# Performance work log

Measured on AMD Instinct MI355X. Metric: run time of the kernel, lower is better.

The kernel has to match this reference:

```python
import jax, jax.numpy as jnp
import numpy as np

H = 16        # attention heads
KVH = 4       # kv heads (GQA)
D = 128       # qk head_dim = qk_nope(64) + qk_rope(64)
ROPE = 64     # rotary sub-dim
VCH = 128     # v_channels
HID = 2048    # hidden size
E = 8         # routed experts
K = 2         # top-k
EPS = 1e-6
THETA = 10000.0


def rmsnorm(x, w):
    return x * jax.lax.rsqrt(jnp.mean(x * x, axis=-1, keepdims=True) + EPS) * w


def apply_rope(x, pos):
    # x: [T, h, ROPE]; rotate-half convention on the rope sub-dim
    half = ROPE // 2
    inv_freq = 1.0 / (THETA ** (jnp.arange(half, dtype=jnp.float32) / half))
    ang = pos.astype(jnp.float32)[:, None] * inv_freq          # [T, half]
    cos = jnp.cos(ang)[:, None, :]
    sin = jnp.sin(ang)[:, None, :]
    x1, x2 = x[..., :half], x[..., half:]
    return jnp.concatenate([x1 * cos - x2 * sin, x1 * sin + x2 * cos], axis=-1)


def swiglu(x, w_gate, w_up, w_down):
    return (jax.nn.silu(x @ w_gate) * (x @ w_up)) @ w_down


def setup_inputs() -> dict:
    key = jax.random.key(0)
    ks = jax.random.split(key, 16)
    T = 2048
    sc = 0.02
    n = lambda k, s: jax.random.normal(k, s, dtype=jnp.float32) * sc
    return {
        "x": jax.random.normal(ks[0], (T, HID), dtype=jnp.float32),
        "positions": jnp.arange(T, dtype=jnp.int32),
        "ln1_w": jnp.ones((HID,), jnp.float32),
        "qkv_w": n(ks[1], (HID, H * D + KVH * D + KVH * VCH)),
        "qkv_b": n(ks[2], (H * D + KVH * D + KVH * VCH,)),
        "k_ln_w": jnp.ones((D,), jnp.float32),
        "o_w": n(ks[3], (H * VCH, HID)),
        "ln2_w": jnp.ones((HID,), jnp.float32),
        "router_w": n(ks[4], (HID, E)),
        "w1": n(ks[5], (E, HID, 512)),
        "w2": n(ks[6], (E, 512, HID)),
        "w3": n(ks[7], (E, HID, 512)),
        "sw1": n(ks[8], (HID, 1024)),
        "sw2": n(ks[9], (1024, HID)),
        "sw3": n(ks[10], (HID, 1024)),
    }


def reference(x, positions, ln1_w, qkv_w, qkv_b, k_ln_w, o_w, ln2_w,
              router_w, w1, w2, w3, sw1, sw2, sw3):
    T = x.shape[0]
    # --- attention block ---
    h = rmsnorm(x, ln1_w)
    qkv = h @ qkv_w + qkv_b
    q = qkv[:, : H * D].reshape(T, H, D)
    k = qkv[:, H * D : H * D + KVH * D].reshape(T, KVH, D)
    v = qkv[:, H * D + KVH * D :].reshape(T, KVH, VCH)
    k = rmsnorm(k, k_ln_w)  # per-head k_layernorm over head_dim
    # rope applied to the trailing qk_rope_dim of q/k
    q = jnp.concatenate([q[..., : D - ROPE], apply_rope(q[..., D - ROPE :], positions)], -1)
    k = jnp.concatenate([k[..., : D - ROPE], apply_rope(k[..., D - ROPE :], positions)], -1)
    rep = H // KVH
    kf = jnp.repeat(k, rep, axis=1)   # [T, H, D]
    vf = jnp.repeat(v, rep, axis=1)   # [T, H, VCH]
    scale = D ** -0.5
    scores = jnp.einsum("qhd,khd->hqk", q, kf) * scale
    causal = jnp.tril(jnp.ones((T, T), dtype=bool))
    scores = jnp.where(causal[None], scores, jnp.float32(-1e30))
    p = jax.nn.softmax(scores, axis=-1)
    attn = jnp.einsum("hqk,khv->qhv", p, vf).reshape(T, H * VCH)
    x = x + attn @ o_w
    # --- MoE block: shared expert + top-k routed experts ---
    h2 = rmsnorm(x, ln2_w)
    probs = jax.nn.softmax(h2 @ router_w, axis=-1)            # [T, E]
    topw, topi = jax.lax.top_k(probs, K)
    topw = topw / jnp.sum(topw, axis=-1, keepdims=True)        # renormalize top-k
    combine = jnp.sum(jax.nn.one_hot(topi, E, dtype=h2.dtype) * topw[..., None], axis=1)  # [T, E]
    moe = swiglu(h2, sw1, sw3, sw2)                            # shared expert
    for e in range(E):  # small fixed expert count
        moe = moe + combine[:, e : e + 1] * swiglu(h2, w1[e], w3[e], w2[e])
    return x + moe
```

## Files before the change

kernel.cpp:

```cpp
#include <hip/hip_runtime.h>


typedef _Float16 half_t;
typedef _Float16 half8 __attribute__((ext_vector_type(8)));
typedef float    f32x4 __attribute__((ext_vector_type(4)));
typedef float    floatx4 __attribute__((ext_vector_type(4)));

#define T_TOK 2048
#define HIDN  2048
#define NH    16
#define NKVH  4
#define HD    128
#define QKV_N 3072
#define NEXP  8

#define MFMA16(a,b,c) __builtin_amdgcn_mfma_f32_16x16x32_f16(a,b,c,0,0,0)

__device__ __forceinline__ void gload_lds16(const half_t* g, half_t* l) {
    __builtin_amdgcn_global_load_lds(
        (const __attribute__((address_space(1))) void*)g,
        (__attribute__((address_space(3))) void*)l, 16, 0, 0);
}

__global__ __launch_bounds__(256)
void rmsnorm_split_k(const float* __restrict__ x, const float* __restrict__ w,
                     half_t* __restrict__ hi, half_t* __restrict__ lo)
{
    const int row = blockIdx.x, tid = threadIdx.x;
    const float* xr = x + (size_t)row * HIDN;
    floatx4 v0 = *(const floatx4*)(xr + tid * 8);
    floatx4 v1 = *(const floatx4*)(xr + tid * 8 + 4);
    float ss = v0[0]*v0[0] + v0[1]*v0[1] + v0[2]*v0[2] + v0[3]*v0[3]
             + v1[0]*v1[0] + v1[1]*v1[1] + v1[2]*v1[2] + v1[3]*v1[3];
    for (int o = 32; o; o >>= 1) ss += __shfl_down(ss, o);
    __shared__ float red[4];
    if ((tid & 63) == 0) red[tid >> 6] = ss;
    __syncthreads();
    ss = red[0] + red[1] + red[2] + red[3];
    float rs = rsqrtf(ss * (1.0f / HIDN) + 1e-6f);
    floatx4 w0 = *(const floatx4*)(w + tid * 8);
    floatx4 w1 = *(const floatx4*)(w + tid * 8 + 4);
    float vv[8] = { v0[0]*w0[0], v0[1]*w0[1], v0[2]*w0[2], v0[3]*w0[3],
                    v1[0]*w1[0], v1[1]*w1[1], v1[2]*w1[2], v1[3]*w1[3] };
    half8 hv, lv;
#pragma unroll
    for (int j = 0; j < 8; ++j) {
        float o = vv[j] * rs;
        half_t h = (half_t)o;
        hv[j] = h;
        lv[j] = (half_t)((o - (float)h) * 1024.0f);
    }
    *(half8*)(hi + (size_t)row * HIDN + tid * 8) = hv;
    if (lo) *(half8*)(lo + (size_t)row * HIDN + tid * 8) = lv;
}

__global__ __launch_bounds__(256)
void transpose_split2(const float* __restrict__ src, half_t* __restrict__ dh,
                      half_t* __restrict__ dl, int sstride, int dstride)
{
    __shared__ float tile[32][36];
    const int n0 = blockIdx.x * 32, k0 = blockIdx.y * 32;
    const int tid = threadIdx.x;
    {
        int r = tid >> 3, c = (tid & 7) * 4;
        *(floatx4*)&tile[r][c] =
            *(const floatx4*)(src + (size_t)(k0 + r) * sstride + n0 + c);
    }
    __syncthreads();
    int n = tid & 31, g = tid >> 5, gg = g & 3;
    half8 hv;
    if (g < 4) {
#pragma unroll
        for (int j = 0; j < 8; ++j) hv[j] = (half_t)tile[gg * 8 + j][n];
        *(half8*)(dh + (size_t)(n0 + n) * dstride + k0 + gg * 8) = hv;
    } else {
#pragma unroll
        for (int j = 0; j < 8; ++j) {
            float v = tile[gg * 8 + j][n];
            half_t h = (half_t)v;
            hv[j] = (half_t)((v - (float)h) * 1024.0f);
        }
        *(half8*)(dl + (size_t)(n0 + n) * dstride + k0 + gg * 8) = hv;
    }
}

__global__ __launch_bounds__(256)
void transpose_f16(const float* __restrict__ src, half_t* __restrict__ dh,
                   int sstride, int dstride)
{
    __shared__ float tile[32][68];
    const int n0 = blockIdx.x * 64, k0 = blockIdx.y * 32;
    const int tid = threadIdx.x;
    {
        int r = tid >> 3, c = (tid & 7) * 4;
        const float* s = src + (size_t)(k0 + r) * sstride + n0;
        *(floatx4*)&tile[r][c]      = *(const floatx4*)(s + c);
        *(floatx4*)&tile[r][c + 32] = *(const floatx4*)(s + c + 32);
    }
    __syncthreads();
    int n = tid & 63, g = tid >> 6;
    half8 hv;
#pragma unroll
    for (int j = 0; j < 8; ++j) hv[j] = (half_t)tile[g * 8 + j][n];
    *(half8*)(dh + (size_t)(n0 + n) * dstride + k0 + g * 8) = hv;
}

__global__ __launch_bounds__(256)
void w13_transpose(const float* __restrict__ sw1, const float* __restrict__ w1,
                   const float* __restrict__ sw3, const float* __restrict__ w3,
                   half_t* __restrict__ dst)
{
    __shared__ float tile[32][68];
    const int n0 = blockIdx.x * 64, k0 = blockIdx.y * 32;
    const int tid = threadIdx.x;
    const float* base;
    int stride;
    if (n0 < 1024)      { base = sw1 + n0; stride = 1024; }
    else if (n0 < 5120) { int e = (n0 - 1024) >> 9;
                          base = w1 + (size_t)e * HIDN * 512 + ((n0 - 1024) & 511);
                          stride = 512; }
    else if (n0 < 6144) { base = sw3 + (n0 - 5120); stride = 1024; }
    else                { int e = (n0 - 6144) >> 9;
                          base = w3 + (size_t)e * HIDN * 512 + ((n0 - 6144) & 511);
                          stride = 512; }
    {
        int r = tid >> 3, c = (tid & 7) * 4;
        const float* s = base + (size_t)(k0 + r) * stride;
        *(floatx4*)&tile[r][c]      = *(const floatx4*)(s + c);
        *(floatx4*)&tile[r][c + 32] = *(const floatx4*)(s + c + 32);
    }
    __syncthreads();
    int n = tid & 63, g = tid >> 6;
    half8 hv;
#pragma unroll
    for (int j = 0; j < 8; ++j) hv[j] = (half_t)tile[g * 8 + j][n];
    *(half8*)(dst + (size_t)(n0 + n) * HIDN + k0 + g * 8) = hv;
}

__global__ __launch_bounds__(256)
void w2_transpose(const float* __restrict__ sw2, const float* __restrict__ w2,
                  half_t* __restrict__ dst)
{
    __shared__ float tile[32][68];
    const int n0 = blockIdx.x * 64, k0 = blockIdx.y * 32;
    const int tid = threadIdx.x;
    {
        int r = tid >> 3, c = (tid & 7) * 4;
        int k = k0 + r;
        const float* s;
        if (k < 1024) s = sw2 + (size_t)k * HIDN + n0;
        else {
            int e = (k - 1024) >> 9, kk = (k - 1024) & 511;
            s = w2 + ((size_t)e * 512 + kk) * HIDN + n0;
        }
        *(floatx4*)&tile[r][c]      = *(const floatx4*)(s + c);
        *(floatx4*)&tile[r][c + 32] = *(const floatx4*)(s + c + 32);
    }
    __syncthreads();
    int n = tid & 63, g = tid >> 6;
    half8 hv;
#pragma unroll
    for (int j = 0; j < 8; ++j) hv[j] = (half_t)tile[g * 8 + j][n];
    *(half8*)(dst + (size_t)(n0 + n) * 5120 + k0 + g * 8) = hv;
}

__global__ __launch_bounds__(256)
void owu_kernel(const float* __restrict__ ow, const float* __restrict__ ln2w,
                const float* __restrict__ rw, float* __restrict__ owu)
{
    const int k = blockIdx.x * 4 + (threadIdx.x >> 6);
    const int lane = threadIdx.x & 63;
    float acc[NEXP] = {};
    const float* row = ow + (size_t)k * HIDN;
#pragma unroll
    for (int j = 0; j < 8; ++j) {
        int c = j * 256 + lane * 4;
        floatx4 ov = *(const floatx4*)(row + c);
        floatx4 lw = *(const floatx4*)(ln2w + c);
#pragma unroll
        for (int i = 0; i < 4; ++i) {
            float s = ov[i] * lw[i];
            const float* rwc = rw + (size_t)(c + i) * NEXP;
#pragma unroll
            for (int e = 0; e < NEXP; ++e) acc[e] += s * rwc[e];
        }
    }
#pragma unroll
    for (int e = 0; e < NEXP; ++e)
        for (int o = 32; o; o >>= 1) acc[e] += __shfl_down(acc[e], o);
    if (lane == 0) {
#pragma unroll
        for (int e = 0; e < NEXP; ++e) owu[(size_t)k * NEXP + e] = acc[e];
    }
}

template<bool SPLIT, int BM>
__global__ __launch_bounds__(256, 2)
void gemm_f16(const half_t* __restrict__ Ah, const half_t* __restrict__ Al,
              const half_t* __restrict__ Bth, const half_t* __restrict__ Btl,
              const float* __restrict__ bias, const float* __restrict__ res,
              float* __restrict__ Cf, half_t* __restrict__ Ch,
              int M, int N, int K)
{
    constexpr int NBUF = SPLIT ? 2 : 1;
    constexpr int MR = BM / 32;
    __shared__ half_t As[2][NBUF][BM * 32];
    __shared__ half_t Bs[2][NBUF][128 * 32];
    const int tid = threadIdx.x, lane = tid & 63, wid = tid >> 6;
    const int l15 = lane & 15, l4 = lane >> 4;
    const int row0 = blockIdx.y * BM, col0 = blockIdx.x * 128;
    const int wr = (wid >> 1) * (BM / 2), wc = (wid & 1) * 64;
    f32x4 accM[MR][4] = {}, accC[MR][4] = {};
    const int lrw = lane >> 2, lcl = (lane & 3) * 8;

#define STAGE(BUF, K0)                                                        \
    do {                                                                      \
        _Pragma("unroll")                                                     \
        for (int j = 0; j < BM / 64; ++j) {                                   \
            const int r = wid * (BM / 4) + j * 16;                            \
            const size_t ga = (size_t)(row0 + r + lrw) * K + (K0) + lcl;      \
            gload_lds16(Ah + ga, &As[BUF][0][r * 32]);                        \
            if constexpr (SPLIT) gload_lds16(Al + ga, &As[BUF][1][r * 32]);   \
        }                                                                     \
        _Pragma("unroll")                                                     \
        for (int j = 0; j < 2; ++j) {                                         \
            const int r = wid * 32 + j * 16;                                  \
            const size_t gb = (size_t)(col0 + r + lrw) * K + (K0) + lcl;      \
            gload_lds16(Bth + gb, &Bs[BUF][0][r * 32]);                       \
            if constexpr (SPLIT) gload_lds16(Btl + gb, &Bs[BUF][1][r * 32]);  \
        }                                                                     \
    } while (0)

    STAGE(0, 0);
    __syncthreads();
    int cur = 0;
    for (int k0 = 0; k0 < K; k0 += 32, cur ^= 1) {
        if (k0 + 32 < K) STAGE(cur ^ 1, k0 + 32);
        half8 ah[MR], al[MR], bh[4], bl[4];
#pragma unroll
        for (int m = 0; m < MR; ++m) {
            int off = (wr + m * 16 + l15) * 32 + l4 * 8;
            ah[m] = *(const half8*)&As[cur][0][off];
            if constexpr (SPLIT) al[m] = *(const half8*)&As[cur][1][off];
        }
#pragma unroll
        for (int n = 0; n < 4; ++n) {
            int off = (wc + n * 16 + l15) * 32 + l4 * 8;
            bh[n] = *(const half8*)&Bs[cur][0][off];
            if constexpr (SPLIT) bl[n] = *(const half8*)&Bs[cur][1][off];
        }
#pragma unroll
        for (int m = 0; m < MR; ++m)
#pragma unroll
            for (int n = 0; n < 4; ++n) {
                accM[m][n] = MFMA16(ah[m], bh[n], accM[m][n]);
                if constexpr (SPLIT) {
                    accC[m][n] = MFMA16(ah[m], bl[n], accC[m][n]);
                    accC[m][n] = MFMA16(al[m], bh[n], accC[m][n]);
                }
            }
        __syncthreads();
    }
#undef STAGE

#pragma unroll
    for (int m = 0; m < MR; ++m) {
#pragma unroll
        for (int n = 0; n < 4; ++n) {
            int gr0 = row0 + wr + m * 16 + l4 * 4;
            int gc  = col0 + wc + n * 16 + l15;
            float b = bias ? bias[gc] : 0.0f;
#pragma unroll
            for (int i = 0; i < 4; ++i) {
                float v = accM[m][n][i];
                if constexpr (SPLIT) v += accC[m][n][i] * (1.0f / 1024.0f);
                v += b;
                size_t idx = (size_t)(gr0 + i) * N + gc;
                if (res) v += res[idx];
                if (Cf) Cf[idx] = v;
                if (Ch) Ch[idx] = (half_t)v;
            }
        }
    }
}

__global__ __launch_bounds__(256)
void qkv_prep(const float* __restrict__ qkv, const int* __restrict__ pos,
              const float* __restrict__ klnw,
              half_t* __restrict__ qh, half_t* __restrict__ ql,
              half_t* __restrict__ kh, half_t* __restrict__ kl)
{
    const int t = blockIdx.x, tid = threadIdx.x, lane = tid & 63, wid = tid >> 6;
    const float* row = qkv + (size_t)t * QKV_N;
    __shared__ float cs[32], sn[32];
    if (tid < 32) {
        double freq = exp((double)tid * -0.28782313662425572);
        double ang = (double)pos[t] * freq;
        const double twopi = 6.283185307179586476925286766559;
        ang -= twopi * floor(ang * (1.0 / twopi));
        float a = (float)ang;
        cs[tid] = cosf(a);
        sn[tid] = sinf(a);
    }
    __syncthreads();

    const float qscale = 0.08838834764831845f;
    {
        const int hh = tid >> 4, d0 = (tid & 15) * 8;
        const float* qrow = row + hh * HD;
        float outv[8];
        if (d0 < 64) {
#pragma unroll
            for (int j = 0; j < 8; ++j) outv[j] = qrow[d0 + j];
        } else if (d0 < 96) {
            int j0 = d0 - 64;
#pragma unroll
            for (int j = 0; j < 8; ++j) {
                int jj = j0 + j;
                outv[j] = qrow[64 + jj] * cs[jj] - qrow[96 + jj] * sn[jj];
            }
        } else {
            int j0 = d0 - 96;
#pragma unroll
            for (int j = 0; j < 8; ++j) {
                int jj = j0 + j;
                outv[j] = qrow[64 + jj] * sn[jj] + qrow[96 + jj] * cs[jj];
            }
        }
        half8 hv, lv;
#pragma unroll
        for (int j = 0; j < 8; ++j) {
            float o = outv[j] * qscale;
            half_t h = (half_t)o;
            hv[j] = h;
            lv[j] = (half_t)((o - (float)h) * 1024.0f);
        }
        size_t base = (size_t)t * (NH * HD) + hh * HD + d0;
        *(half8*)(qh + base) = hv;
        *(half8*)(ql + base) = lv;
    }
    {
        const float* krow = row + NH * HD + wid * HD;
        float a0 = krow[lane], a1 = krow[64 + lane];
        float ss = a0 * a0 + a1 * a1;
        for (int o = 32; o; o >>= 1) ss += __shfl_down(ss, o);
        ss = __shfl(ss, 0);
        float rs = rsqrtf(ss * (1.0f / HD) + 1e-6f);
        float n0 = a0 * rs * klnw[lane];
        float n1 = a1 * rs * klnw[64 + lane];
        float other = __shfl_xor(n1, 32);
        int j = lane & 31;
        float o1 = (lane < 32) ? (n1 * cs[j] - other * sn[j])
                               : (other * sn[j] + n1 * cs[j]);
        size_t base = (size_t)t * (NKVH * HD) + wid * HD;
        half_t h;
        h = (half_t)n0; kh[base + lane] = h;
        kl[base + lane] = (half_t)((n0 - (float)h) * 1024.0f);
        h = (half_t)o1; kh[base + 64 + lane] = h;
        kl[base + 64 + lane] = (half_t)((o1 - (float)h) * 1024.0f);
    }
}

__global__ __launch_bounds__(256, 2)
void attn_kernel(const half_t* __restrict__ qh, const half_t* __restrict__ ql,
                 const half_t* __restrict__ kh, const half_t* __restrict__ kl,
                 const half_t* __restrict__ vth, const half_t* __restrict__ vtl,
                 half_t* __restrict__ oh, half_t* __restrict__ ol,
                 float* __restrict__ Op0, float* __restrict__ Op1,
                 float* __restrict__ ml)
{
    const int bid = blockIdx.x;
    const int h = bid & 15, r = bid >> 4;
    int q, c;
    if (r < 8)       { q = r;                 c = 0; }
    else if (r < 24) { q = 8 + ((r - 8) >> 1);  c = (r - 8) & 1; }
    else if (r < 48) { q = 16 + (r - 24) / 3;   c = (r - 24) % 3; }
    else             { q = 24 + ((r - 48) >> 2); c = (r - 48) & 3; }
    const int nch = (q < 8) ? 1 : (q < 16) ? 2 : (q < 24) ? 3 : 4;
    const int kvbeg = c * 512;
    const int kvend = min(kvbeg + 512, q * 64 + 64);

    const int kvh = h >> 2;
    const int tid = threadIdx.x, lane = tid & 63, wid = tid >> 6;
    const int q0 = q * 64 + wid * 16;
    const int l15 = lane & 15, l4 = lane >> 4;

    __shared__ half_t Ksh[32][136], Ksl[32][136];
    __shared__ half_t Vsh[128][40], Vsl[128][40];
    __shared__ half_t Ph[4][16][40], Pl[4][16][40];

    half8 qfh[4], qfl[4];
    {
        const size_t qb = (size_t)(q0 + l15) * (NH * HD) + h * HD + l4 * 8;
#pragma unroll
        for (int cc = 0; cc < 4; ++cc) {
            qfh[cc] = *(const half8*)(qh + qb + cc * 32);
            qfl[cc] = *(const half8*)(ql + qb + cc * 32);
        }
    }

    f32x4 om[8] = {}, oc[8] = {};
    float mrow[4] = { -1e30f, -1e30f, -1e30f, -1e30f };
    float lrow[4] = {};

    const int kr = tid >> 4, kc = (tid & 15) * 8;
    const int vd = tid >> 2, vc = (tid & 3) * 8;
    uint4 rk0h, rk1h, rk0l, rk1l, rv0h, rv1h, rv0l, rv1l;

#define LOAD_TILE(KV0)                                                        \
    do {                                                                      \
        size_t sk0 = (size_t)((KV0) + kr) * (NKVH * HD) + kvh * HD + kc;      \
        size_t sk1 = sk0 + (size_t)16 * (NKVH * HD);                          \
        rk0h = *(const uint4*)(kh + sk0);  rk0l = *(const uint4*)(kl + sk0);  \
        rk1h = *(const uint4*)(kh + sk1);  rk1l = *(const uint4*)(kl + sk1);  \
        size_t sv0 = (size_t)(kvh * HD + vd) * T_TOK + (KV0) + vc;            \
        size_t sv1 = sv0 + (size_t)64 * T_TOK;                                \
        rv0h = *(const uint4*)(vth + sv0); rv0l = *(const uint4*)(vtl + sv0); \
        rv1h = *(const uint4*)(vth + sv1); rv1l = *(const uint4*)(vtl + sv1); \
    } while (0)

    LOAD_TILE(kvbeg);
    for (int kv0 = kvbeg; kv0 < kvend; kv0 += 32) {
        *(uint4*)&Ksh[kr][kc]      = rk0h;  *(uint4*)&Ksl[kr][kc]      = rk0l;
        *(uint4*)&Ksh[kr + 16][kc] = rk1h;  *(uint4*)&Ksl[kr + 16][kc] = rk1l;
        *(uint4*)&Vsh[vd][vc]      = rv0h;  *(uint4*)&Vsl[vd][vc]      = rv0l;
        *(uint4*)&Vsh[vd + 64][vc] = rv1h;  *(uint4*)&Vsl[vd + 64][vc] = rv1l;
        __syncthreads();
        if (kv0 + 32 < kvend) LOAD_TILE(kv0 + 32);

        f32x4 sf[2];
        __builtin_amdgcn_s_setprio(1);
#pragma unroll
        for (int t2 = 0; t2 < 2; ++t2) {
            f32x4 s = {}, sc = {};
#pragma unroll
            for (int cc = 0; cc < 4; ++cc) {
                half8 bh = *(const half8*)&Ksh[t2 * 16 + l15][cc * 32 + l4 * 8];
                half8 bl = *(const half8*)&Ksl[t2 * 16 + l15][cc * 32 + l4 * 8];
                s  = MFMA16(qfh[cc], bh, s);
                sc = MFMA16(qfh[cc], bl, sc);
                sc = MFMA16(qfl[cc], bh, sc);
            }
            sf[t2] = s + sc * (1.0f / 1024.0f);
        }
        __builtin_amdgcn_s_setprio(0);

        float pmax[4];
#pragma unroll
        for (int i = 0; i < 4; ++i) {
            const int qg = q0 + l4 * 4 + i;
#pragma unroll
            for (int t2 = 0; t2 < 2; ++t2) {
                int kvg = kv0 + t2 * 16 + l15;
                if (kvg > qg) sf[t2][i] = -1e30f;
            }
            float mx = fmaxf(sf[0][i], sf[1][i]);
#pragma unroll
            for (int o = 1; o < 16; o <<= 1) mx = fmaxf(mx, __shfl_xor(mx, o));
            pmax[i] = mx;
        }
        float dm = fmaxf(fmaxf(pmax[0] - mrow[0], pmax[1] - mrow[1]),
                         fmaxf(pmax[2] - mrow[2], pmax[3] - mrow[3]));
        if (__any(dm > 6.0f)) {
#pragma unroll
            for (int i = 0; i < 4; ++i) {
                float mnew = fmaxf(mrow[i], pmax[i]);
                float resc = expf(mrow[i] - mnew);
                lrow[i] *= resc;
#pragma unroll
                for (int c8 = 0; c8 < 8; ++c8) {
                    om[c8][i] *= resc; oc[c8][i] *= resc;
                }
                mrow[i] = mnew;
            }
        }
#pragma unroll
        for (int i = 0; i < 4; ++i) {
            float p0 = expf(sf[0][i] - mrow[i]);
            float p1 = expf(sf[1][i] - mrow[i]);
            lrow[i] += p0 + p1;
            half_t hh;
            hh = (half_t)p0;
            Ph[wid][l4 * 4 + i][l15] = hh;
            Pl[wid][l4 * 4 + i][l15] = (half_t)((p0 - (float)hh) * 1024.0f);
            hh = (half_t)p1;
            Ph[wid][l4 * 4 + i][16 + l15] = hh;
            Pl[wid][l4 * 4 + i][16 + l15] = (half_t)((p1 - (float)hh) * 1024.0f);
        }

        half8 pah = *(const half8*)&Ph[wid][l15][l4 * 8];
        half8 pal = *(const half8*)&Pl[wid][l15][l4 * 8];
        __builtin_amdgcn_s_setprio(1);
#pragma unroll
        for (int c8 = 0; c8 < 8; ++c8) {
            half8 vh = *(const half8*)&Vsh[c8 * 16 + l15][l4 * 8];
            half8 vl = *(const half8*)&Vsl[c8 * 16 + l15][l4 * 8];
            om[c8] = MFMA16(pah, vh, om[c8]);
            oc[c8] = MFMA16(pah, vl, oc[c8]);
            oc[c8] = MFMA16(pal, vh, oc[c8]);
        }
        __builtin_amdgcn_s_setprio(0);
        __syncthreads();
    }
#undef LOAD_TILE

#pragma unroll
    for (int i = 0; i < 4; ++i)
#pragma unroll
        for (int o = 1; o < 16; o <<= 1) lrow[i] += __shfl_xor(lrow[i], o);

    if (nch == 1) {
#pragma unroll
        for (int c8 = 0; c8 < 8; ++c8) {
#pragma unroll
            for (int i = 0; i < 4; ++i) {
                float v = (om[c8][i] + oc[c8][i] * (1.0f / 1024.0f)) / lrow[i];
                size_t idx = (size_t)(q0 + l4 * 4 + i) * (NH * HD) + h * HD
                           + c8 * 16 + l15;
                half_t hh = (half_t)v;
                oh[idx] = hh;
                ol[idx] = (half_t)((v - (float)hh) * 1024.0f);
            }
        }
    } else {
        float* Op = (bid < 768) ? Op0 + (size_t)bid * 8192
                                : Op1 + (size_t)(bid - 768) * 8192;
#pragma unroll
        for (int c8 = 0; c8 < 8; ++c8) {
#pragma unroll
            for (int i = 0; i < 4; ++i) {
                int row64 = wid * 16 + l4 * 4 + i;
                Op[row64 * 128 + c8 * 16 + l15] =
                    om[c8][i] + oc[c8][i] * (1.0f / 1024.0f);
            }
        }
        if (l15 == 0) {
#pragma unroll
            for (int i = 0; i < 4; ++i) {
                int row64 = wid * 16 + l4 * 4 + i;
                ml[(size_t)bid * 128 + row64]      = mrow[i];
                ml[(size_t)bid * 128 + 64 + row64] = lrow[i];
            }
        }
    }
}

__global__ __launch_bounds__(256)
void attn_combine(const float* __restrict__ Op0, const float* __restrict__ Op1,
                  const float* __restrict__ ml,
                  half_t* __restrict__ oh, half_t* __restrict__ ol)
{
    const int bid = blockIdx.x;
    const int h = bid & 15, q = 8 + (bid >> 4);
    const int nch = (q < 16) ? 2 : (q < 24) ? 3 : 4;
    const int r0 = (q < 16) ? 8 + (q - 8) * 2
                 : (q < 24) ? 24 + (q - 16) * 3
                            : 48 + (q - 24) * 4;
    const int tid = threadIdx.x;
    const int row = tid >> 2, cg = (tid & 3) * 32;

    const float* Oc[4];
    float m[4], lv[4];
#pragma unroll
    for (int c = 0; c < 4; ++c) {
        int cc = (c < nch) ? c : nch - 1;
        int slot = (r0 + cc) * 16 + h;
        const float* base = (slot < 768) ? Op0 + (size_t)slot * 8192
                                         : Op1 + (size_t)(slot - 768) * 8192;
        Oc[c] = base + row * 128 + cg;
        m[c]  = ml[(size_t)slot * 128 + row];
        lv[c] = (c < nch) ? ml[(size_t)slot * 128 + 64 + row] : 0.0f;
    }
    float M = fmaxf(fmaxf(m[0], m[1]), fmaxf(m[2], m[3]));
    float w[4], wsum = 0.0f;
#pragma unroll
    for (int c = 0; c < 4; ++c) { w[c] = expf(m[c] - M); wsum += lv[c] * w[c]; }
    float inv = 1.0f / wsum;
    float wO[4];
#pragma unroll
    for (int c = 0; c < 4; ++c) wO[c] = (c < nch) ? w[c] * inv : 0.0f;

    size_t obase = (size_t)(q * 64 + row) * (NH * HD) + h * HD + cg;
#pragma unroll
    for (int jj = 0; jj < 4; ++jj) {
        floatx4 a0 = {0,0,0,0}, a1 = {0,0,0,0};
#pragma unroll
        for (int c = 0; c < 4; ++c) {
            floatx4 v0 = *(const floatx4*)(Oc[c] + jj * 8);
            floatx4 v1 = *(const floatx4*)(Oc[c] + jj * 8 + 4);
            a0 += wO[c] * v0;
            a1 += wO[c] * v1;
        }
        half8 hv, lvv;
#pragma unroll
        for (int k = 0; k < 4; ++k) {
            half_t hh = (half_t)a0[k];
            hv[k] = hh; lvv[k] = (half_t)((a0[k] - (float)hh) * 1024.0f);
            hh = (half_t)a1[k];
            hv[4 + k] = hh; lvv[4 + k] = (half_t)((a1[k] - (float)hh) * 1024.0f);
        }
        *(half8*)(oh + obase + jj * 8) = hv;
        *(half8*)(ol + obase + jj * 8) = lvv;
    }
}

__global__ __launch_bounds__(256)
void router_linear(const float* __restrict__ x, const half_t* __restrict__ ah,
                   const half_t* __restrict__ al, const float* __restrict__ x2,
                   const float* __restrict__ ln2w, const float* __restrict__ rw,
                   const float* __restrict__ owu, float* __restrict__ combine)
{
    const int t = blockIdx.x, tid = threadIdx.x;
    const float* xr2 = x2 + (size_t)t * HIDN;
    float ss = 0.0f;
#pragma unroll
    for (int i = 0; i < 8; ++i) {
        float v = xr2[tid + i * 256];
        ss += v * v;
    }
    for (int o = 32; o; o >>= 1) ss += __shfl_down(ss, o);
    __shared__ float red[4];
    if ((tid & 63) == 0) red[tid >> 6] = ss;
    __syncthreads();
    ss = red[0] + red[1] + red[2] + red[3];
    float rs = rsqrtf(ss * (1.0f / HIDN) + 1e-6f);

    const float* xr = x + (size_t)t * HIDN;
    const half_t* ar = ah + (size_t)t * HIDN;
    const half_t* alr = al + (size_t)t * HIDN;
    float acc[NEXP] = {};
#pragma unroll
    for (int i = 0; i < 8; ++i) {
        int c = tid + i * 256;
        float xv = xr[c] * ln2w[c];
        float ap = (float)ar[c] + (float)alr[c] * (1.0f / 1024.0f);
        const float* rwc = rw + (size_t)c * NEXP;
        const float* owc = owu + (size_t)c * NEXP;
#pragma unroll
        for (int e = 0; e < NEXP; ++e) acc[e] += xv * rwc[e] + ap * owc[e];
    }
#pragma unroll
    for (int e = 0; e < NEXP; ++e)
        for (int o = 32; o; o >>= 1) acc[e] += __shfl_down(acc[e], o);
    __shared__ float red8[4][NEXP];
    if ((tid & 63) == 0)
#pragma unroll
        for (int e = 0; e < NEXP; ++e) red8[tid >> 6][e] = acc[e];
    __syncthreads();
    if (tid == 0) {
        float lg[NEXP];
#pragma unroll
        for (int e = 0; e < NEXP; ++e)
            lg[e] = (red8[0][e] + red8[1][e] + red8[2][e] + red8[3][e]) * rs;
        int i1 = 0;
        for (int e = 1; e < NEXP; ++e) if (lg[e] > lg[i1]) i1 = e;
        int i2 = (i1 == 0) ? 1 : 0;
        for (int e = 0; e < NEXP; ++e) if (e != i1 && lg[e] > lg[i2]) i2 = e;
        float mx = lg[i1];
        float p1 = expf(lg[i1] - mx), p2 = expf(lg[i2] - mx);
        float inv = 1.0f / (p1 + p2);
        float* cr = combine + (size_t)t * NEXP;
#pragma unroll
        for (int e = 0; e < NEXP; ++e) cr[e] = 0.0f;
        cr[i1] = p1 * inv;
        cr[i2] = p2 * inv;
    }
}

__global__ __launch_bounds__(256)
void moe_act(const half_t* __restrict__ GU, const float* __restrict__ comb,
             half_t* __restrict__ Abig)
{
    int idx = blockIdx.x * 256 + threadIdx.x;
    int t = idx / 640, c8 = idx % 640;
    int n = c8 * 8;
    half8 g8 = *(const half8*)(GU + (size_t)t * 10240 + n);
    half8 u8 = *(const half8*)(GU + (size_t)t * 10240 + 5120 + n);
    float sc = (n < 1024) ? 1.0f : comb[(size_t)t * NEXP + ((n - 1024) >> 9)];
    half8 o8;
#pragma unroll
    for (int j = 0; j < 8; ++j) {
        float g = (float)g8[j], u = (float)u8[j];
        float s = g / (1.0f + expf(-g));
        o8[j] = (half_t)(s * u * sc);
    }
    *(half8*)(Abig + (size_t)t * 5120 + n) = o8;
}

extern "C" void kernel_launch(void* const* d_in, const int* in_sizes, int n_in,
                              void* d_out, int out_size, void* d_ws, size_t ws_size,
                              hipStream_t stream)
{
    (void)in_sizes; (void)n_in; (void)out_size; (void)ws_size;
    const float* x    = (const float*)d_in[0];
    const int*   pos  = (const int*)  d_in[1];
    const float* ln1w = (const float*)d_in[2];
    const float* qkvw = (const float*)d_in[3];
    const float* qkvb = (const float*)d_in[4];
    const float* klnw = (const float*)d_in[5];
    const float* ow   = (const float*)d_in[6];
    const float* ln2w = (const float*)d_in[7];
    const float* rw   = (const float*)d_in[8];
    const float* w1   = (const float*)d_in[9];
    const float* w2   = (const float*)d_in[10];
    const float* w3   = (const float*)d_in[11];
    const float* sw1  = (const float*)d_in[12];
    const float* sw2  = (const float*)d_in[13];
    const float* sw3  = (const float*)d_in[14];
    float* out = (float*)d_out;

    char* ws = (char*)d_ws;
    const size_t AB = 16842752;
    float*  x2      = (float*)(ws);
    float*  combine = (float*)(ws + 16777216);
    half_t* h_hi    = (half_t*)(ws + AB);
    half_t* h_lo    = (half_t*)(ws + AB + 8388608);
    half_t* qkvwt_h = (half_t*)(ws + AB + 16777216);
    half_t* qkvwt_l = (half_t*)(ws + AB + 29360128);
    float*  qkv     = (float*)(ws + AB + 41943040);
    half_t* q_h     = (half_t*)(ws + AB + 67108864);
    half_t* q_l     = (half_t*)(ws + AB + 75497472);
    half_t* k_h     = (half_t*)(ws + AB + 83886080);
    half_t* k_l     = (half_t*)(ws + AB + 85983232);
    half_t* vt_h    = (half_t*)(ws + AB + 88080384);
    half_t* vt_l    = (half_t*)(ws + AB + 90177536);
    half_t* attn_h  = (half_t*)(ws + AB);
    half_t* attn_l  = (half_t*)(ws + AB + 8388608);
    half_t* owt     = (half_t*)(ws + AB + 16777216);
    float*  ow_u    = (float*)(ws + AB + 25165824);
    float*  mlpart  = (float*)(ws + AB + 25231360);
    float*  Opart0  = (float*)(ws + AB + 41943040);
    float*  Opart1  = (float*)(ws);
    half_t* h2      = (half_t*)(ws + AB + 33554432);
    half_t* W13t    = (half_t*)(ws + AB + 41943040);
    half_t* GU      = (half_t*)(ws + AB + 83886080);
    half_t* Abig    = (half_t*)(ws + AB);
    half_t* W2t     = (half_t*)(ws + AB + 41943040);

    dim3 b256(256);

    rmsnorm_split_k<<<T_TOK, b256, 0, stream>>>(x, ln1w, h_hi, h_lo);
    transpose_split2<<<dim3(QKV_N / 32, HIDN / 32), b256, 0, stream>>>(
        qkvw, qkvwt_h, qkvwt_l, QKV_N, HIDN);
    gemm_f16<true, 64><<<dim3(QKV_N / 128, T_TOK / 64), b256, 0, stream>>>(
        h_hi, h_lo, qkvwt_h, qkvwt_l, qkvb, nullptr, qkv, nullptr,
        T_TOK, QKV_N, HIDN);
    qkv_prep<<<T_TOK, b256, 0, stream>>>(qkv, pos, klnw, q_h, q_l, k_h, k_l);
    transpose_split2<<<dim3(512 / 32, T_TOK / 32), b256, 0, stream>>>(
        qkv + 2560, vt_h, vt_l, QKV_N, T_TOK);
    transpose_f16<<<dim3(HIDN / 64, HIDN / 32), b256, 0, stream>>>(
        ow, owt, HIDN, HIDN);
    owu_kernel<<<512, b256, 0, stream>>>(ow, ln2w, rw, ow_u);
    attn_kernel<<<1280, b256, 0, stream>>>(
        q_h, q_l, k_h, k_l, vt_h, vt_l, attn_h, attn_l,
        Opart0, Opart1, mlpart);
    attn_combine<<<384, b256, 0, stream>>>(Opart0, Opart1, mlpart,
                                           attn_h, attn_l);
    gemm_f16<false, 64><<<dim3(HIDN / 128, T_TOK / 64), b256, 0, stream>>>(
        attn_h, nullptr, owt, nullptr, nullptr, x, x2, nullptr,
        T_TOK, HIDN, HIDN);
    router_linear<<<T_TOK, b256, 0, stream>>>(
        x, attn_h, attn_l, x2, ln2w, rw, ow_u, combine);
    rmsnorm_split_k<<<T_TOK, b256, 0, stream>>>(x2, ln2w, h2, nullptr);
    w13_transpose<<<dim3(10240 / 64, HIDN / 32), b256, 0, stream>>>(
        sw1, w1, sw3, w3, W13t);
    gemm_f16<false, 128><<<dim3(10240 / 128, T_TOK / 128), b256, 0, stream>>>(
        h2, nullptr, W13t, nullptr, nullptr, nullptr, nullptr, GU,
        T_TOK, 10240, HIDN);
    w2_transpose<<<dim3(HIDN / 64, 5120 / 32), b256, 0, stream>>>(sw2, w2, W2t);
    moe_act<<<(T_TOK * 640) / 256, b256, 0, stream>>>(GU, combine, Abig);
    gemm_f16<false, 64><<<dim3(HIDN / 128, T_TOK / 64), b256, 0, stream>>>(
        Abig, nullptr, W2t, nullptr, nullptr, x2, out, nullptr,
        T_TOK, HIDN, 5120);
}
```

Before: 650.6 us.

## Replace dense all-expert MoE with sparse grouped GEMMs over routed token pairs

Instead of running every expert's gate/up and down projections over all tokens and scaling by a mostly-zero combine matrix, the router now emits top-k indices, counts tokens per expert, scans offsets and scatters token-expert pairs into per-expert padded groups. Grouped GEMM kernels then compute gate/up and down projections only for the routed pairs, and a final kernel adds the two expert outputs into the result. The shared expert keeps its dense GEMMs, now separate and with a leading-dimension parameter. Attention chunk boundaries are also rebalanced evenly across splits. This removes about three quarters of the routed-expert FLOPs, at the cost of several small launches, atomics and a gather of the token rows.

```diff
diff --git a/kernel.cpp b/kernel.cpp
--- a/kernel.cpp
+++ b/kernel.cpp
@@ -13,6 +13,7 @@
 #define HD    128
 #define QKV_N 3072
 #define NEXP  8
+#define NPAIR_MAX 4608
 
 #define MFMA16(a,b,c) __builtin_amdgcn_mfma_f32_16x16x32_f16(a,b,c,0,0,0)
 
@@ -20,6 +21,10 @@
     __builtin_amdgcn_global_load_lds(
         (const __attribute__((address_space(1))) void*)g,
         (__attribute__((address_space(3))) void*)l, 16, 0, 0);
+}
+
+__device__ __forceinline__ float silu_f(float g) {
+    return g / (1.0f + expf(-g));
 }
 
 __global__ __launch_bounds__(256)
@@ -116,10 +121,10 @@
     const float* base;
     int stride;
     if (n0 < 1024)      { base = sw1 + n0; stride = 1024; }
-    else if (n0 < 5120) { int e = (n0 - 1024) >> 9;
-                          base = w1 + (size_t)e * HIDN * 512 + ((n0 - 1024) & 511);
+    else if (n0 < 2048) { base = sw3 + (n0 - 1024); stride = 1024; }
+    else if (n0 < 6144) { int e = (n0 - 2048) >> 9;
+                          base = w1 + (size_t)e * HIDN * 512 + ((n0 - 2048) & 511);
                           stride = 512; }
-    else if (n0 < 6144) { base = sw3 + (n0 - 5120); stride = 1024; }
     else                { int e = (n0 - 6144) >> 9;
                           base = w3 + (size_t)e * HIDN * 512 + ((n0 - 6144) & 511);
                           stride = 512; }
@@ -200,7 +205,7 @@
               const half_t* __restrict__ Bth, const half_t* __restrict__ Btl,
               const float* __restrict__ bias, const float* __restrict__ res,
               float* __restrict__ Cf, half_t* __restrict__ Ch,
-              int M, int N, int K)
+              int M, int N, int K, int ldb)
 {
     constexpr int NBUF = SPLIT ? 2 : 1;
     constexpr int MR = BM / 32;
@@ -225,7 +230,7 @@
         _Pragma("unroll")                                                     \
         for (int j = 0; j < 2; ++j) {                                         \
             const int r = wid * 32 + j * 16;                                  \
-            const size_t gb = (size_t)(col0 + r + lrw) * K + (K0) + lcl;      \
+            const size_t gb = (size_t)(col0 + r + lrw) * ldb + (K0) + lcl;    \
             gload_lds16(Bth + gb, &Bs[BUF][0][r * 32]);                       \
             if constexpr (SPLIT) gload_lds16(Btl + gb, &Bs[BUF][1][r * 32]);  \
         }                                                                     \
@@ -282,6 +287,133 @@
             }
         }
     }
+}
+
+__global__ __launch_bounds__(256, 2)
+void gemm_grouped_gu(const half_t* __restrict__ h2, const half_t* __restrict__ W13t,
+                     const int* __restrict__ pairTok, const int* __restrict__ basep,
+                     half_t* __restrict__ GUp)
+{
+    __shared__ half_t As[2][64 * 32];
+    __shared__ half_t Bs[2][128 * 32];
+    const int tid = threadIdx.x, lane = tid & 63, wid = tid >> 6;
+    const int l15 = lane & 15, l4 = lane >> 4;
+    const int lrw = lane >> 2, lcl = (lane & 3) * 8;
+    const int row0 = blockIdx.y * 64, ct = blockIdx.x;
+    int e = 0;
+#pragma unroll
+    for (int i = 1; i < NEXP; ++i) if (row0 >= basep[i]) e = i;
+    const int brow0 = (ct < 4) ? (2048 + 512 * e + ct * 128)
+                               : (6144 + 512 * e + (ct - 4) * 128);
+    const int wr = (wid >> 1) * 32, wc = (wid & 1) * 64;
+    const int tok = pairTok[row0 + wid * 16 + lrw];
+    const half_t* Abase = h2 + (size_t)tok * HIDN + lcl;
+    f32x4 acc[2][4] = {};
+
+#define GSTAGE(BUF, K0)                                                       \
+    do {                                                                      \
+        gload_lds16(Abase + (K0), &As[BUF][(wid * 16) * 32]);                 \
+        _Pragma("unroll")                                                     \
+        for (int j = 0; j < 2; ++j) {                                         \
+            const int r = wid * 32 + j * 16;                                  \
+            const size_t gb = (size_t)(brow0 + r + lrw) * HIDN + (K0) + lcl;  \
+            gload_lds16(W13t + gb, &Bs[BUF][r * 32]);                         \
+        }                                                                     \
+    } while (0)
+
+    GSTAGE(0, 0);
+    __syncthreads();
+    int cur = 0;
+    for (int k0 = 0; k0 < HIDN; k0 += 32, cur ^= 1) {
+        if (k0 + 32 < HIDN) GSTAGE(cur ^ 1, k0 + 32);
+        half8 ah[2], bh[4];
+#pragma unroll
+        for (int m = 0; m < 2; ++m)
+            ah[m] = *(const half8*)&As[cur][(wr + m * 16 + l15) * 32 + l4 * 8];
+#pragma unroll
+        for (int n = 0; n < 4; ++n)
+            bh[n] = *(const half8*)&Bs[cur][(wc + n * 16 + l15) * 32 + l4 * 8];
+#pragma unroll
+        for (int m = 0; m < 2; ++m)
+#pragma unroll
+            for (int n = 0; n < 4; ++n)
+                acc[m][n] = MFMA16(ah[m], bh[n], acc[m][n]);
+        __syncthreads();
+    }
+#undef GSTAGE
+
+#pragma unroll
+    for (int m = 0; m < 2; ++m)
+#pragma unroll
+        for (int n = 0; n < 4; ++n) {
+            int gr0 = row0 + wr + m * 16 + l4 * 4;
+            int gc  = ct * 128 + wc + n * 16 + l15;
+#pragma unroll
+            for (int i = 0; i < 4; ++i)
+                GUp[(size_t)(gr0 + i) * 1024 + gc] = (half_t)acc[m][n][i];
+        }
+}
+
+__global__ __launch_bounds__(256, 2)
+void gemm_grouped_down(const half_t* __restrict__ Ab, const half_t* __restrict__ W2t,
+                       const int* __restrict__ basep, half_t* __restrict__ Ypair)
+{
+    __shared__ half_t As[2][64 * 32];
+    __shared__ half_t Bs[2][128 * 32];
+    const int tid = threadIdx.x, lane = tid & 63, wid = tid >> 6;
+    const int l15 = lane & 15, l4 = lane >> 4;
+    const int lrw = lane >> 2, lcl = (lane & 3) * 8;
+    const int row0 = blockIdx.y * 64, col0 = blockIdx.x * 128;
+    int e = 0;
+#pragma unroll
+    for (int i = 1; i < NEXP; ++i) if (row0 >= basep[i]) e = i;
+    const int bcol = 1024 + 512 * e;
+    const int wr = (wid >> 1) * 32, wc = (wid & 1) * 64;
+    f32x4 acc[2][4] = {};
+
+#define DSTAGE(BUF, K0)                                                       \
+    do {                                                                      \
+        const size_t ga = (size_t)(row0 + wid * 16 + lrw) * 512 + (K0) + lcl; \
+        gload_lds16(Ab + ga, &As[BUF][(wid * 16) * 32]);                      \
+        _Pragma("unroll")                                                     \
+        for (int j = 0; j < 2; ++j) {                                         \
+            const int r = wid * 32 + j * 16;                                  \
+            const size_t gb = (size_t)(col0 + r + lrw) * 5120 + bcol + (K0) + lcl; \
+            gload_lds16(W2t + gb, &Bs[BUF][r * 32]);                          \
+        }                                                                     \
+    } while (0)
+
+    DSTAGE(0, 0);
+    __syncthreads();
+    int cur = 0;
+    for (int k0 = 0; k0 < 512; k0 += 32, cur ^= 1) {
+        if (k0 + 32 < 512) DSTAGE(cur ^ 1, k0 + 32);
+        half8 ah[2], bh[4];
+#pragma unroll
+        for (int m = 0; m < 2; ++m)
+            ah[m] = *(const half8*)&As[cur][(wr + m * 16 + l15) * 32 + l4 * 8];
+#pragma unroll
+        for (int n = 0; n < 4; ++n)
+            bh[n] = *(const half8*)&Bs[cur][(wc + n * 16 + l15) * 32 + l4 * 8];
+#pragma unroll
+        for (int m = 0; m < 2; ++m)
+#pragma unroll
+            for (int n = 0; n < 4; ++n)
+                acc[m][n] = MFMA16(ah[m], bh[n], acc[m][n]);
+        __syncthreads();
+    }
+#undef DSTAGE
+
+#pragma unroll
+    for (int m = 0; m < 2; ++m)
+#pragma unroll
+        for (int n = 0; n < 4; ++n) {
+            int gr0 = row0 + wr + m * 16 + l4 * 4;
+            int gc  = col0 + wc + n * 16 + l15;
+#pragma unroll
+            for (int i = 0; i < 4; ++i)
+                Ypair[(size_t)(gr0 + i) * HIDN + gc] = (half_t)acc[m][n][i];
+        }
 }
 
 __global__ __launch_bounds__(256)
@@ -377,8 +509,9 @@
     else if (r < 48) { q = 16 + (r - 24) / 3;   c = (r - 24) % 3; }
     else             { q = 24 + ((r - 48) >> 2); c = (r - 48) & 3; }
     const int nch = (q < 8) ? 1 : (q < 16) ? 2 : (q < 24) ? 3 : 4;
-    const int kvbeg = c * 512;
-    const int kvend = min(kvbeg + 512, q * 64 + 64);
+    const int nt = 2 * (q + 1);
+    const int kvbeg = ((c * nt) / nch) * 32;
+    const int kvend = (((c + 1) * nt) / nch) * 32;
 
     const int kvh = h >> 2;
     const int tid = threadIdx.x, lane = tid & 63, wid = tid >> 6;
@@ -608,7 +741,9 @@
 void router_linear(const float* __restrict__ x, const half_t* __restrict__ ah,
                    const half_t* __restrict__ al, const float* __restrict__ x2,
                    const float* __restrict__ ln2w, const float* __restrict__ rw,
-                   const float* __restrict__ owu, float* __restrict__ combine)
+                   const float* __restrict__ owu,
+                   int* __restrict__ topi, float* __restrict__ topv,
+                   int* __restrict__ cnt)
 {
     const int t = blockIdx.x, tid = threadIdx.x;
     const float* xr2 = x2 + (size_t)t * HIDN;
@@ -659,32 +794,100 @@
         float mx = lg[i1];
         float p1 = expf(lg[i1] - mx), p2 = expf(lg[i2] - mx);
         float inv = 1.0f / (p1 + p2);
-        float* cr = combine + (size_t)t * NEXP;
-#pragma unroll
-        for (int e = 0; e < NEXP; ++e) cr[e] = 0.0f;
-        cr[i1] = p1 * inv;
-        cr[i2] = p2 * inv;
-    }
-}
-
-__global__ __launch_bounds__(256)
-void moe_act(const half_t* __restrict__ GU, const float* __restrict__ comb,
-             half_t* __restrict__ Abig)
+        topi[2 * t] = i1;     topi[2 * t + 1] = i2;
+        topv[2 * t] = p1 * inv; topv[2 * t + 1] = p2 * inv;
+        atomicAdd(&cnt[i1], 1);
+        atomicAdd(&cnt[i2], 1);
+    }
+}
+
+__global__ __launch_bounds__(256)
+void moe_init(int* __restrict__ cnt, int* __restrict__ pairTok,
+              float* __restrict__ pairW)
 {
     int idx = blockIdx.x * 256 + threadIdx.x;
-    int t = idx / 640, c8 = idx % 640;
-    int n = c8 * 8;
-    half8 g8 = *(const half8*)(GU + (size_t)t * 10240 + n);
-    half8 u8 = *(const half8*)(GU + (size_t)t * 10240 + 5120 + n);
-    float sc = (n < 1024) ? 1.0f : comb[(size_t)t * NEXP + ((n - 1024) >> 9)];
+    if (idx < NPAIR_MAX) { pairTok[idx] = 0; pairW[idx] = 0.0f; }
+    if (idx < NEXP) cnt[idx] = 0;
+}
+
+__global__ __launch_bounds__(64)
+void moe_scan(const int* __restrict__ cnt, int* __restrict__ fill,
+              int* __restrict__ basep)
+{
+    if (threadIdx.x == 0) {
+        int acc = 0;
+        for (int e = 0; e < NEXP; ++e) {
+            basep[e] = acc;
+            fill[e] = acc;
+            acc += (cnt[e] + 63) & ~63;
+        }
+        basep[NEXP] = acc;
+    }
+}
+
+__global__ __launch_bounds__(256)
+void moe_scatter(const int* __restrict__ topi, const float* __restrict__ topv,
+                 int* __restrict__ fill, int* __restrict__ pairTok,
+                 float* __restrict__ pairW, int* __restrict__ pairPos)
+{
+    int t = blockIdx.x * 256 + threadIdx.x;
+#pragma unroll
+    for (int j = 0; j < 2; ++j) {
+        int e = topi[2 * t + j];
+        int pos = atomicAdd(&fill[e], 1);
+        pairTok[pos] = t;
+        pairW[pos] = topv[2 * t + j];
+        pairPos[2 * t + j] = pos;
+    }
+}
+
+__global__ __launch_bounds__(256)
+void act_shared(const half_t* __restrict__ GUs, half_t* __restrict__ As)
+{
+    int idx = blockIdx.x * 256 + threadIdx.x;
+    int t = idx >> 7, c = (idx & 127) * 8;
+    half8 g8 = *(const half8*)(GUs + (size_t)t * 2048 + c);
+    half8 u8 = *(const half8*)(GUs + (size_t)t * 2048 + 1024 + c);
     half8 o8;
 #pragma unroll
-    for (int j = 0; j < 8; ++j) {
-        float g = (float)g8[j], u = (float)u8[j];
-        float s = g / (1.0f + expf(-g));
-        o8[j] = (half_t)(s * u * sc);
-    }
-    *(half8*)(Abig + (size_t)t * 5120 + n) = o8;
+    for (int j = 0; j < 8; ++j)
+        o8[j] = (half_t)(silu_f((float)g8[j]) * (float)u8[j]);
+    *(half8*)(As + (size_t)t * 1024 + c) = o8;
+}
+
+__global__ __launch_bounds__(256)
+void act_sparse(const half_t* __restrict__ GUp, const float* __restrict__ pairW,
+                half_t* __restrict__ Ab)
+{
+    int idx = blockIdx.x * 256 + threadIdx.x;
+    int p = idx >> 6, c = (idx & 63) * 8;
+    half8 g8 = *(const half8*)(GUp + (size_t)p * 1024 + c);
+    half8 u8 = *(const half8*)(GUp + (size_t)p * 1024 + 512 + c);
+    float w = pairW[p];
+    half8 o8;
+#pragma unroll
+    for (int j = 0; j < 8; ++j)
+        o8[j] = (half_t)(silu_f((float)g8[j]) * (float)u8[j] * w);
+    *(half8*)(Ab + (size_t)p * 512 + c) = o8;
+}
+
+__global__ __launch_bounds__(256)
+void moe_final(const half_t* __restrict__ Ypair, const int* __restrict__ pairPos,
+               float* __restrict__ out)
+{
+    int t = blockIdx.x, c0 = threadIdx.x * 8;
+    int p1 = pairPos[2 * t], p2 = pairPos[2 * t + 1];
+    half8 y1 = *(const half8*)(Ypair + (size_t)p1 * HIDN + c0);
+    half8 y2 = *(const half8*)(Ypair + (size_t)p2 * HIDN + c0);
+    float* o = out + (size_t)t * HIDN + c0;
+    floatx4 a = *(floatx4*)o, b = *(floatx4*)(o + 4);
+#pragma unroll
+    for (int j = 0; j < 4; ++j) {
+        a[j] += (float)y1[j] + (float)y2[j];
+        b[j] += (float)y1[4 + j] + (float)y2[4 + j];
+    }
+    *(floatx4*)o = a;
+    *(floatx4*)(o + 4) = b;
 }
 
 extern "C" void kernel_launch(void* const* d_in, const int* in_sizes, int n_in,
@@ -712,7 +915,6 @@
     char* ws = (char*)d_ws;
     const size_t AB = 16842752;
     float*  x2      = (float*)(ws);
-    float*  combine = (float*)(ws + 16777216);
     half_t* h_hi    = (half_t*)(ws + AB);
     half_t* h_lo    = (half_t*)(ws + AB + 8388608);
     half_t* qkvwt_h = (half_t*)(ws + AB + 16777216);
@@ -728,14 +930,25 @@
     half_t* attn_l  = (half_t*)(ws + AB + 8388608);
     half_t* owt     = (half_t*)(ws + AB + 16777216);
     float*  ow_u    = (float*)(ws + AB + 25165824);
+    int*    cnt     = (int*)(ws + AB + 25231360);
+    int*    fill    = cnt + 16;
+    int*    basep   = cnt + 32;
+    int*    topi    = cnt + 64;
+    float*  topv    = (float*)(cnt + 4160);
+    int*    pairPos = (int*)(cnt + 8256);
+    int*    pairTok = (int*)(cnt + 12352);
+    float*  pairW   = (float*)(cnt + 16960);
     float*  mlpart  = (float*)(ws + AB + 25231360);
     float*  Opart0  = (float*)(ws + AB + 41943040);
     float*  Opart1  = (float*)(ws);
     half_t* h2      = (half_t*)(ws + AB + 33554432);
     half_t* W13t    = (half_t*)(ws + AB + 41943040);
-    half_t* GU      = (half_t*)(ws + AB + 83886080);
-    half_t* Abig    = (half_t*)(ws + AB);
+    half_t* GUs     = (half_t*)(ws + AB + 83886080);
+    half_t* As_sh   = (half_t*)(ws + AB);
+    half_t* GUp     = (half_t*)(ws + AB + 4194304);
+    half_t* Ab      = (half_t*)(ws + AB + 16777216);
     half_t* W2t     = (half_t*)(ws + AB + 41943040);
+    half_t* Ypair   = (half_t*)(ws + AB + 92274688);
 
     dim3 b256(256);
 
@@ -744,7 +957,7 @@
         qkvw, qkvwt_h, qkvwt_l, QKV_N, HIDN);
     gemm_f16<true, 64><<<dim3(QKV_N / 128, T_TOK / 64), b256, 0, stream>>>(
         h_hi, h_lo, qkvwt_h, qkvwt_l, qkvb, nullptr, qkv, nullptr,
-        T_TOK, QKV_N, HIDN);
+        T_TOK, QKV_N, HIDN, HIDN);
     qkv_prep<<<T_TOK, b256, 0, stream>>>(qkv, pos, klnw, q_h, q_l, k_h, k_l);
     transpose_split2<<<dim3(512 / 32, T_TOK / 32), b256, 0, stream>>>(
         qkv + 2560, vt_h, vt_l, QKV_N, T_TOK);
@@ -758,18 +971,28 @@
                                            attn_h, attn_l);
     gemm_f16<false, 64><<<dim3(HIDN / 128, T_TOK / 64), b256, 0, stream>>>(
         attn_h, nullptr, owt, nullptr, nullptr, x, x2, nullptr,
-        T_TOK, HIDN, HIDN);
+        T_TOK, HIDN, HIDN, HIDN);
+    moe_init<<<18, b256, 0, stream>>>(cnt, pairTok, pairW);
     router_linear<<<T_TOK, b256, 0, stream>>>(
-        x, attn_h, attn_l, x2, ln2w, rw, ow_u, combine);
+        x, attn_h, attn_l, x2, ln2w, rw, ow_u, topi, topv, cnt);
+    moe_scan<<<1, 64, 0, stream>>>(cnt, fill, basep);
+    moe_scatter<<<NEXP, b256, 0, stream>>>(topi, topv, fill,
+                                           pairTok, pairW, pairPos);
     rmsnorm_split_k<<<T_TOK, b256, 0, stream>>>(x2, ln2w, h2, nullptr);
     w13_transpose<<<dim3(10240 / 64, HIDN / 32), b256, 0, stream>>>(
         sw1, w1, sw3, w3, W13t);
-    gemm_f16<false, 128><<<dim3(10240 / 128, T_TOK / 128), b256, 0, stream>>>(
-        h2, nullptr, W13t, nullptr, nullptr, nullptr, nullptr, GU,
-        T_TOK, 10240, HIDN);
+    gemm_f16<false, 64><<<dim3(2048 / 128, T_TOK / 64), b256, 0, stream>>>(
+        h2, nullptr, W13t, nullptr, nullptr, nullptr, nullptr, GUs,
+        T_TOK, 2048, HIDN, HIDN);
+    gemm_grouped_gu<<<dim3(8, NPAIR_MAX / 64), b256, 0, stream>>>(
+        h2, W13t, pairTok, basep, GUp);
+    act_shared<<<(T_TOK * 128) / 256, b256, 0, stream>>>(GUs, As_sh);
+    act_sparse<<<(NPAIR_MAX * 64) / 256, b256, 0, stream>>>(GUp, pairW, Ab);
     w2_transpose<<<dim3(HIDN / 64, 5120 / 32), b256, 0, stream>>>(sw2, w2, W2t);
-    moe_act<<<(T_TOK * 640) / 256, b256, 0, stream>>>(GU, combine, Abig);
     gemm_f16<false, 64><<<dim3(HIDN / 128, T_TOK / 64), b256, 0, stream>>>(
-        Abig, nullptr, W2t, nullptr, nullptr, x2, out, nullptr,
-        T_TOK, HIDN, 5120);
-}
+        As_sh, nullptr, W2t, nullptr, nullptr, x2, out, nullptr,
+        T_TOK, HIDN, 1024, 5120);
+    gemm_grouped_down<<<dim3(16, NPAIR_MAX / 64), b256, 0, stream>>>(
+        Ab, W2t, basep, Ypair);
+    moe_final<<<T_TOK, b256, 0, stream>>>(Ypair, pairPos, out);
+}
```

New measurement: 622.2 us. 1.05x faster.
